# Kernel optimization log

Measured on AMD Instinct MI355X. Metric: run time of the kernel, lower is better.

Reference implementation:

```python
import jax, jax.numpy as jnp
import numpy as np

B, T, C, H = 8, 2048, 768, 64  # batch, seq_len, embedding_dim, head_size


def setup_inputs() -> dict:
    key = jax.random.key(0)
    k1, k2, k3, k4 = jax.random.split(key, 4)
    x = jax.random.normal(k1, (B, T, C), dtype=jnp.float32)
    attention_mask = jnp.ones((B, T), dtype=jnp.float32)
    # nn.Linear(C, H, bias=False) weights stored pre-transposed as (C, H)
    scale = 0.02
    Wq = jax.random.normal(k2, (C, H), dtype=jnp.float32) * scale
    Wk = jax.random.normal(k3, (C, H), dtype=jnp.float32) * scale
    Wv = jax.random.normal(k4, (C, H), dtype=jnp.float32) * scale
    return {"x": x, "attention_mask": attention_mask, "Wq": Wq, "Wk": Wk, "Wv": Wv}


def reference(x, attention_mask, Wq, Wk, Wv):
    # x: [B,T,C]; attention_mask: [B,T] (multiplied per query row)
    head_size = Wq.shape[-1]
    q = x @ Wq  # [B,T,H]
    k = x @ Wk  # [B,T,H]
    v = x @ Wv  # [B,T,H]
    inv_sqrt_h = jnp.asarray(1.0 / np.sqrt(head_size), x.dtype)
    s = jnp.einsum('bqh,bkh->bqk', q, k) * inv_sqrt_h  # [B,T,T]
    # attention_mask.unsqueeze(2) * qK ; masked_fill(qK == 0, -inf)
    s = attention_mask[:, :, None] * s
    s = jnp.where(s == 0, -jnp.inf, s)
    # causal tril mask
    seq = x.shape[1]
    tril = jnp.tril(jnp.ones((seq, seq), dtype=bool))
    s = jnp.where(tril[None, :, :], s, -jnp.inf)
    p = jax.nn.softmax(s, axis=-1)
    # dropout p=0.0 -> identity; nan cleanup (fully-masked rows)
    p = jnp.where(jnp.isnan(p), jnp.asarray(0.0, p.dtype), p)
    out = jnp.einsum('bqk,bkh->bqh', p, v)  # [B,T,H]
    return out
```

## Files before the change

kernel.cpp:

```cpp
#include <hip/hip_runtime.h>
#include <hip/hip_bf16.h>

#define B_ 8
#define T_ 2048
#define C_ 768
#define H_ 64
#define BT_ (B_*T_)

typedef __attribute__((ext_vector_type(8))) short bf16x8;
typedef __attribute__((ext_vector_type(4))) float f32x4;

__device__ __forceinline__ unsigned short f2bf(float x) {
    __hip_bfloat16 h = __float2bfloat16(x);
    return __builtin_bit_cast(unsigned short, h);
}

__device__ __forceinline__ bf16x8 cvt8(float4 a, float4 b) {
    bf16x8 r;
    r[0] = (short)f2bf(a.x); r[1] = (short)f2bf(a.y);
    r[2] = (short)f2bf(a.z); r[3] = (short)f2bf(a.w);
    r[4] = (short)f2bf(b.x); r[5] = (short)f2bf(b.y);
    r[6] = (short)f2bf(b.z); r[7] = (short)f2bf(b.w);
    return r;
}

__global__ __launch_bounds__(256) void wprep(
    const float* __restrict__ Wq, const float* __restrict__ Wk,
    const float* __restrict__ Wv, unsigned short* __restrict__ WTf)
{
    __shared__ float tile[32][68];
    const int bid = blockIdx.x;
    const int m = bid / 24, gc = bid % 24;
    const float* __restrict__ W = (m == 0) ? Wq : (m == 1) ? Wk : Wv;
    const int t = threadIdx.x;
    {
        const int r = t >> 3, c0 = (t & 7) * 8;
        float4 a = *(const float4*)(W + (size_t)(gc * 32 + r) * H_ + c0);
        float4 b = *(const float4*)(W + (size_t)(gc * 32 + r) * H_ + c0 + 4);
        *(float4*)&tile[r][c0]     = a;
        *(float4*)&tile[r][c0 + 4] = b;
    }
    __syncthreads();
    const int fl = t >> 6, lane = t & 63;
    const int q16 = lane & 15, quad = lane >> 4;
    const int f = m * 4 + fl;
    ushort4 u0, u1;
    u0.x = f2bf(tile[quad * 8 + 0][fl * 16 + q16]);
    u0.y = f2bf(tile[quad * 8 + 1][fl * 16 + q16]);
    u0.z = f2bf(tile[quad * 8 + 2][fl * 16 + q16]);
    u0.w = f2bf(tile[quad * 8 + 3][fl * 16 + q16]);
    u1.x = f2bf(tile[quad * 8 + 4][fl * 16 + q16]);
    u1.y = f2bf(tile[quad * 8 + 5][fl * 16 + q16]);
    u1.z = f2bf(tile[quad * 8 + 6][fl * 16 + q16]);
    u1.w = f2bf(tile[quad * 8 + 7][fl * 16 + q16]);
    unsigned short* __restrict__ dst = WTf + ((size_t)(gc * 12 + f) * 64 + lane) * 8;
    *(ushort4*)(dst)     = u0;
    *(ushort4*)(dst + 4) = u1;
}

__global__ __launch_bounds__(256) void qkv_kernel(
    const float* __restrict__ x, const unsigned short* __restrict__ WTf,
    unsigned short* __restrict__ qF, unsigned short* __restrict__ kF,
    unsigned short* __restrict__ vF)
{
    __shared__ __align__(16) unsigned short xS[16 * 772];
    const int tid  = threadIdx.x;
    const int w    = tid >> 6;
    const int lane = tid & 63;
    const int q16  = lane & 15, quad = lane >> 4;
    const int rowBase = blockIdx.x << 4;

    {
        const int r = tid >> 4, l = tid & 15;
        const float* __restrict__ xrow = x + (size_t)(rowBase + r) * C_;
        #pragma unroll
        for (int i = 0; i < 6; i++) {
            const int j = i * 16 + l;
            float4 a = *(const float4*)(xrow + j * 8);
            float4 b = *(const float4*)(xrow + j * 8 + 4);
            *(bf16x8*)&xS[(size_t)r * 772 + j * 8] = cvt8(a, b);
        }
    }
    __syncthreads();

    const int f0 = w * 3;
    const unsigned short* __restrict__ xrowS = xS + q16 * 772 + quad * 8;
    f32x4 acc[3] = {};
    #pragma unroll
    for (int c = 0; c < 24; c++) {
        const unsigned short* __restrict__ wpc =
            WTf + ((size_t)(c * 12 + f0)) * 512 + lane * 8;
        bf16x8 xf = *(const bf16x8*)(xrowS + c * 32);
        bf16x8 w0 = *(const bf16x8*)(wpc);
        bf16x8 w1 = *(const bf16x8*)(wpc + 512);
        bf16x8 w2 = *(const bf16x8*)(wpc + 1024);
        acc[0] = __builtin_amdgcn_mfma_f32_16x16x32_bf16(w0, xf, acc[0], 0, 0, 0);
        acc[1] = __builtin_amdgcn_mfma_f32_16x16x32_bf16(w1, xf, acc[1], 0, 0, 0);
        acc[2] = __builtin_amdgcn_mfma_f32_16x16x32_bf16(w2, xf, acc[2], 0, 0, 0);
    }

    const size_t gt = (size_t)(rowBase >> 4);
    #pragma unroll
    for (int j = 0; j < 3; j++) {
        const int f = f0 + j;
        if (f < 8) {
            ushort4 u;
            u.x = f2bf(acc[j][0]); u.y = f2bf(acc[j][1]);
            u.z = f2bf(acc[j][2]); u.w = f2bf(acc[j][3]);
            const int n4 = f & 3;
            const int qp = (2 * n4 + (quad >> 1)) & 3;
            const int j0 = (quad & 1) * 4;
            unsigned short* __restrict__ dst = (f < 4) ? qF : kF;
            *(ushort4*)(dst + ((gt * 2 + (n4 >> 1)) * 64 + q16 + 16 * qp) * 8 + j0) = u;
        } else {
            const size_t g32 = gt >> 1;
            const int qv = ((int)gt & 1) * 2 + (q16 >> 3);
            const int jv = q16 & 7;
            #pragma unroll
            for (int r = 0; r < 4; r++)
                vF[((g32 * 4 + (f - 8)) * 64 + quad * 4 + r + 16 * qv) * 8 + jv] =
                    f2bf(acc[j][r]);
        }
    }
}

__global__ __launch_bounds__(256) void attn_kernel(
    const unsigned short* __restrict__ qF, const unsigned short* __restrict__ kF,
    const unsigned short* __restrict__ vF, const float* __restrict__ mask,
    float* __restrict__ out)
{
    __shared__ __align__(16) unsigned short pS[4][16][88];
    __shared__ float oS[3][64][17];

    const int tid  = threadIdx.x;
    const int w    = tid >> 6;
    const int lane = tid & 63;
    const int q16  = lane & 15;
    const int quad = lane >> 4;
    const int bid  = blockIdx.x;
    const int b    = bid & 7;
    const int qt   = 127 - (bid >> 3);
    const int qrow = (qt << 4) + q16;

    const size_t qbase = ((size_t)(b * 128 + qt) * 2) * 512 + lane * 8;
    bf16x8 qf0 = *(const bf16x8*)(qF + qbase);
    bf16x8 qf1 = *(const bf16x8*)(qF + qbase + 512);
    const float mrow  = mask[b * T_ + qrow];
    const float maskv = mrow * 0.125f * 1.44269504f;

    f32x4 o[4] = {};
    float l_run = 0.f;

    const int niter = ((qt << 4) + 16 + 63) >> 6;
    const int dt    = niter - 1;

    bf16x8 kf[8], vf[8];
    auto loadK = [&](int kt_) {
        #pragma unroll
        for (int sub = 0; sub < 4; sub++) {
            const unsigned short* kp = kF + ((size_t)(b * 128 + kt_ * 4 + sub) * 2) * 512 + lane * 8;
            kf[2 * sub]     = *(const bf16x8*)(kp);
            kf[2 * sub + 1] = *(const bf16x8*)(kp + 512);
        }
    };
    auto loadV = [&](int kt_) {
        #pragma unroll
        for (int ht = 0; ht < 4; ht++) {
            const unsigned short* vp = vF + ((size_t)(b * 64 + kt_ * 2) * 4 + ht) * 512 + lane * 8;
            vf[2 * ht]     = *(const bf16x8*)(vp);
            vf[2 * ht + 1] = *(const bf16x8*)(vp + 4 * 512);
        }
    };

    if (w < niter) { loadK(w); loadV(w); }

    for (int kt = w; kt < niter; kt += 4) {
        const int kbase = kt << 6;
        const bool more = (kt + 4 < niter);

        f32x4 sa[4] = {};
        #pragma unroll
        for (int sub = 0; sub < 4; sub++) {
            sa[sub] = __builtin_amdgcn_mfma_f32_16x16x32_bf16(kf[2 * sub],     qf0, sa[sub], 0, 0, 0);
            sa[sub] = __builtin_amdgcn_mfma_f32_16x16x32_bf16(kf[2 * sub + 1], qf1, sa[sub], 0, 0, 0);
        }
        if (more) loadK(kt + 4);

        float p[16];
        if (kt != dt) {
            #pragma unroll
            for (int e = 0; e < 16; e++)
                p[e] = __builtin_amdgcn_exp2f(sa[e >> 2][e & 3] * maskv);
        } else {
            #pragma unroll
            for (int sub = 0; sub < 4; sub++)
                #pragma unroll
                for (int r = 0; r < 4; r++) {
                    int kidx = kbase + sub * 16 + quad * 4 + r;
                    float sv = sa[sub][r] * maskv;
                    sv = (kidx > qrow) ? -__builtin_inff() : sv;
                    p[sub * 4 + r] = __builtin_amdgcn_exp2f(sv);
                }
        }
        float psum = (((p[0] + p[1]) + (p[2] + p[3])) + ((p[4] + p[5]) + (p[6] + p[7])))
                   + (((p[8] + p[9]) + (p[10] + p[11])) + ((p[12] + p[13]) + (p[14] + p[15])));
        l_run += psum;

        #pragma unroll
        for (int sub = 0; sub < 4; sub++) {
            unsigned int lo = (unsigned int)f2bf(p[sub * 4 + 0]) | ((unsigned int)f2bf(p[sub * 4 + 1]) << 16);
            unsigned int hi = (unsigned int)f2bf(p[sub * 4 + 2]) | ((unsigned int)f2bf(p[sub * 4 + 3]) << 16);
            *(uint2*)&pS[w][q16][sub * 16 + quad * 4] = make_uint2(lo, hi);
        }
        bf16x8 pf0 = *(const bf16x8*)&pS[w][q16][quad * 8];
        bf16x8 pf1 = *(const bf16x8*)&pS[w][q16][32 + quad * 8];

        #pragma unroll
        for (int ht = 0; ht < 4; ht++) {
            o[ht] = __builtin_amdgcn_mfma_f32_16x16x32_bf16(vf[2 * ht],     pf0, o[ht], 0, 0, 0);
            o[ht] = __builtin_amdgcn_mfma_f32_16x16x32_bf16(vf[2 * ht + 1], pf1, o[ht], 0, 0, 0);
        }
        if (more) loadV(kt + 4);
    }

    l_run += __shfl_xor(l_run, 16);
    l_run += __shfl_xor(l_run, 32);

    if (w > 0) {
        #pragma unroll
        for (int ht = 0; ht < 4; ht++)
            #pragma unroll
            for (int r = 0; r < 4; r++) oS[w - 1][lane][ht * 4 + r] = o[ht][r];
        oS[w - 1][lane][16] = l_run;
    }
    __syncthreads();
    if (w == 0) {
        #pragma unroll
        for (int j = 0; j < 3; j++) {
            #pragma unroll
            for (int ht = 0; ht < 4; ht++)
                #pragma unroll
                for (int r = 0; r < 4; r++) o[ht][r] += oS[j][lane][ht * 4 + r];
            l_run += oS[j][lane][16];
        }
        const float invl = (mrow != 0.f && l_run > 0.f) ? (1.f / l_run) : 0.f;
        #pragma unroll
        for (int ht = 0; ht < 4; ht++) {
            float4 ov = make_float4(o[ht][0] * invl, o[ht][1] * invl,
                                    o[ht][2] * invl, o[ht][3] * invl);
            *(float4*)(out + ((size_t)(b * T_) + qrow) * H_ + ht * 16 + quad * 4) = ov;
        }
    }
}

extern "C" void kernel_launch(void* const* d_in, const int* in_sizes, int n_in,
                              void* d_out, int out_size, void* d_ws, size_t ws_size,
                              hipStream_t stream) {
    const float* x    = (const float*)d_in[0];
    const float* mask = (const float*)d_in[1];
    const float* Wq   = (const float*)d_in[2];
    const float* Wk   = (const float*)d_in[3];
    const float* Wv   = (const float*)d_in[4];
    float* out = (float*)d_out;

    unsigned short* qf = (unsigned short*)d_ws;
    unsigned short* kf = qf + (size_t)BT_ * H_;
    unsigned short* vf = kf + (size_t)BT_ * H_;
    unsigned short* wt = vf + (size_t)BT_ * H_;

    wprep<<<72, 256, 0, stream>>>(Wq, Wk, Wv, wt);
    qkv_kernel<<<BT_ / 16, 256, 0, stream>>>(x, wt, qf, kf, vf);
    attn_kernel<<<B_ * (T_ / 16), 256, 0, stream>>>(qf, kf, vf, mask, out);
}
```

Baseline: 114.8 us.

## Process two 16-row query tiles per block to reuse loaded K/V fragments

Each attention block now handles 32 query rows as two 16-row tiles (A and B) that share the same K and V fragments loaded per iteration, halving K/V global loads per query row. The grid shrinks to half as many blocks. The cost is more registers (two sets of accumulators and scores), fewer blocks for load balancing and occupancy, and tile A doing extra masked work up to tile B's causal length.

```diff
diff --git a/kernel.cpp b/kernel.cpp
--- a/kernel.cpp
+++ b/kernel.cpp
@@ -139,19 +139,26 @@
     const int quad = lane >> 4;
     const int bid  = blockIdx.x;
     const int b    = bid & 7;
-    const int qt   = 127 - (bid >> 3);
-    const int qrow = (qt << 4) + q16;
-
-    const size_t qbase = ((size_t)(b * 128 + qt) * 2) * 512 + lane * 8;
-    bf16x8 qf0 = *(const bf16x8*)(qF + qbase);
-    bf16x8 qf1 = *(const bf16x8*)(qF + qbase + 512);
-    const float mrow  = mask[b * T_ + qrow];
-    const float maskv = mrow * 0.125f * 1.44269504f;
-
-    f32x4 o[4] = {};
-    float l_run = 0.f;
-
-    const int niter = ((qt << 4) + 16 + 63) >> 6;
+    const int g    = 63 - (bid >> 3);
+    const int qtA  = 2 * g, qtB = 2 * g + 1;
+    const int qrowA = (qtA << 4) + q16;
+    const int qrowB = qrowA + 16;
+
+    const size_t qbaseA = ((size_t)(b * 128 + qtA) * 2) * 512 + lane * 8;
+    const size_t qbaseB = ((size_t)(b * 128 + qtB) * 2) * 512 + lane * 8;
+    bf16x8 qfA0 = *(const bf16x8*)(qF + qbaseA);
+    bf16x8 qfA1 = *(const bf16x8*)(qF + qbaseA + 512);
+    bf16x8 qfB0 = *(const bf16x8*)(qF + qbaseB);
+    bf16x8 qfB1 = *(const bf16x8*)(qF + qbaseB + 512);
+    const float mrowA  = mask[b * T_ + qrowA];
+    const float mrowB  = mask[b * T_ + qrowB];
+    const float maskvA = mrowA * 0.125f * 1.44269504f;
+    const float maskvB = mrowB * 0.125f * 1.44269504f;
+
+    f32x4 oA[4] = {}, oB[4] = {};
+    float lA = 0.f, lB = 0.f;
+
+    const int niter = ((qtB << 4) + 16 + 63) >> 6;
     const int dt    = niter - 1;
 
     bf16x8 kf[8], vf[8];
@@ -178,60 +185,122 @@
         const int kbase = kt << 6;
         const bool more = (kt + 4 < niter);
 
-        f32x4 sa[4] = {};
+        f32x4 saA[4] = {}, saB[4] = {};
         #pragma unroll
         for (int sub = 0; sub < 4; sub++) {
-            sa[sub] = __builtin_amdgcn_mfma_f32_16x16x32_bf16(kf[2 * sub],     qf0, sa[sub], 0, 0, 0);
-            sa[sub] = __builtin_amdgcn_mfma_f32_16x16x32_bf16(kf[2 * sub + 1], qf1, sa[sub], 0, 0, 0);
+            saA[sub] = __builtin_amdgcn_mfma_f32_16x16x32_bf16(kf[2 * sub],     qfA0, saA[sub], 0, 0, 0);
+            saA[sub] = __builtin_amdgcn_mfma_f32_16x16x32_bf16(kf[2 * sub + 1], qfA1, saA[sub], 0, 0, 0);
+            saB[sub] = __builtin_amdgcn_mfma_f32_16x16x32_bf16(kf[2 * sub],     qfB0, saB[sub], 0, 0, 0);
+            saB[sub] = __builtin_amdgcn_mfma_f32_16x16x32_bf16(kf[2 * sub + 1], qfB1, saB[sub], 0, 0, 0);
         }
         if (more) loadK(kt + 4);
 
-        float p[16];
-        if (kt != dt) {
-            #pragma unroll
-            for (int e = 0; e < 16; e++)
-                p[e] = __builtin_amdgcn_exp2f(sa[e >> 2][e & 3] * maskv);
-        } else {
-            #pragma unroll
-            for (int sub = 0; sub < 4; sub++)
-                #pragma unroll
-                for (int r = 0; r < 4; r++) {
-                    int kidx = kbase + sub * 16 + quad * 4 + r;
-                    float sv = sa[sub][r] * maskv;
-                    sv = (kidx > qrow) ? -__builtin_inff() : sv;
-                    p[sub * 4 + r] = __builtin_amdgcn_exp2f(sv);
-                }
-        }
-        float psum = (((p[0] + p[1]) + (p[2] + p[3])) + ((p[4] + p[5]) + (p[6] + p[7])))
-                   + (((p[8] + p[9]) + (p[10] + p[11])) + ((p[12] + p[13]) + (p[14] + p[15])));
-        l_run += psum;
-
-        #pragma unroll
-        for (int sub = 0; sub < 4; sub++) {
-            unsigned int lo = (unsigned int)f2bf(p[sub * 4 + 0]) | ((unsigned int)f2bf(p[sub * 4 + 1]) << 16);
-            unsigned int hi = (unsigned int)f2bf(p[sub * 4 + 2]) | ((unsigned int)f2bf(p[sub * 4 + 3]) << 16);
-            *(uint2*)&pS[w][q16][sub * 16 + quad * 4] = make_uint2(lo, hi);
-        }
-        bf16x8 pf0 = *(const bf16x8*)&pS[w][q16][quad * 8];
-        bf16x8 pf1 = *(const bf16x8*)&pS[w][q16][32 + quad * 8];
-
+        {
+            float p[16];
+            if (kt != dt) {
+                #pragma unroll
+                for (int e = 0; e < 16; e++)
+                    p[e] = __builtin_amdgcn_exp2f(saA[e >> 2][e & 3] * maskvA);
+            } else {
+                #pragma unroll
+                for (int sub = 0; sub < 4; sub++)
+                    #pragma unroll
+                    for (int r = 0; r < 4; r++) {
+                        int kidx = kbase + sub * 16 + quad * 4 + r;
+                        float sv = saA[sub][r] * maskvA;
+                        sv = (kidx > qrowA) ? -__builtin_inff() : sv;
+                        p[sub * 4 + r] = __builtin_amdgcn_exp2f(sv);
+                    }
+            }
+            lA += (((p[0] + p[1]) + (p[2] + p[3])) + ((p[4] + p[5]) + (p[6] + p[7])))
+                + (((p[8] + p[9]) + (p[10] + p[11])) + ((p[12] + p[13]) + (p[14] + p[15])));
+            #pragma unroll
+            for (int sub = 0; sub < 4; sub++) {
+                unsigned int lo = (unsigned int)f2bf(p[sub * 4 + 0]) | ((unsigned int)f2bf(p[sub * 4 + 1]) << 16);
+                unsigned int hi = (unsigned int)f2bf(p[sub * 4 + 2]) | ((unsigned int)f2bf(p[sub * 4 + 3]) << 16);
+                *(uint2*)&pS[w][q16][sub * 16 + quad * 4] = make_uint2(lo, hi);
+            }
+            bf16x8 pf0 = *(const bf16x8*)&pS[w][q16][quad * 8];
+            bf16x8 pf1 = *(const bf16x8*)&pS[w][q16][32 + quad * 8];
+            #pragma unroll
+            for (int ht = 0; ht < 4; ht++) {
+                oA[ht] = __builtin_amdgcn_mfma_f32_16x16x32_bf16(vf[2 * ht],     pf0, oA[ht], 0, 0, 0);
+                oA[ht] = __builtin_amdgcn_mfma_f32_16x16x32_bf16(vf[2 * ht + 1], pf1, oA[ht], 0, 0, 0);
+            }
+        }
+
+        {
+            float p[16];
+            if (kt != dt) {
+                #pragma unroll
+                for (int e = 0; e < 16; e++)
+                    p[e] = __builtin_amdgcn_exp2f(saB[e >> 2][e & 3] * maskvB);
+            } else {
+                #pragma unroll
+                for (int sub = 0; sub < 4; sub++)
+                    #pragma unroll
+                    for (int r = 0; r < 4; r++) {
+                        int kidx = kbase + sub * 16 + quad * 4 + r;
+                        float sv = saB[sub][r] * maskvB;
+                        sv = (kidx > qrowB) ? -__builtin_inff() : sv;
+                        p[sub * 4 + r] = __builtin_amdgcn_exp2f(sv);
+                    }
+            }
+            lB += (((p[0] + p[1]) + (p[2] + p[3])) + ((p[4] + p[5]) + (p[6] + p[7])))
+                + (((p[8] + p[9]) + (p[10] + p[11])) + ((p[12] + p[13]) + (p[14] + p[15])));
+            #pragma unroll
+            for (int sub = 0; sub < 4; sub++) {
+                unsigned int lo = (unsigned int)f2bf(p[sub * 4 + 0]) | ((unsigned int)f2bf(p[sub * 4 + 1]) << 16);
+                unsigned int hi = (unsigned int)f2bf(p[sub * 4 + 2]) | ((unsigned int)f2bf(p[sub * 4 + 3]) << 16);
+                *(uint2*)&pS[w][q16][sub * 16 + quad * 4] = make_uint2(lo, hi);
+            }
+            bf16x8 pf0 = *(const bf16x8*)&pS[w][q16][quad * 8];
+            bf16x8 pf1 = *(const bf16x8*)&pS[w][q16][32 + quad * 8];
+            #pragma unroll
+            for (int ht = 0; ht < 4; ht++) {
+                oB[ht] = __builtin_amdgcn_mfma_f32_16x16x32_bf16(vf[2 * ht],     pf0, oB[ht], 0, 0, 0);
+                oB[ht] = __builtin_amdgcn_mfma_f32_16x16x32_bf16(vf[2 * ht + 1], pf1, oB[ht], 0, 0, 0);
+            }
+        }
+        if (more) loadV(kt + 4);
+    }
+
+    lA += __shfl_xor(lA, 16); lA += __shfl_xor(lA, 32);
+    lB += __shfl_xor(lB, 16); lB += __shfl_xor(lB, 32);
+
+    if (w > 0) {
+        #pragma unroll
+        for (int ht = 0; ht < 4; ht++)
+            #pragma unroll
+            for (int r = 0; r < 4; r++) oS[w - 1][lane][ht * 4 + r] = oA[ht][r];
+        oS[w - 1][lane][16] = lA;
+    }
+    __syncthreads();
+    if (w == 0) {
+        #pragma unroll
+        for (int j = 0; j < 3; j++) {
+            #pragma unroll
+            for (int ht = 0; ht < 4; ht++)
+                #pragma unroll
+                for (int r = 0; r < 4; r++) oA[ht][r] += oS[j][lane][ht * 4 + r];
+            lA += oS[j][lane][16];
+        }
+        const float invl = (mrowA != 0.f && lA > 0.f) ? (1.f / lA) : 0.f;
         #pragma unroll
         for (int ht = 0; ht < 4; ht++) {
-            o[ht] = __builtin_amdgcn_mfma_f32_16x16x32_bf16(vf[2 * ht],     pf0, o[ht], 0, 0, 0);
-            o[ht] = __builtin_amdgcn_mfma_f32_16x16x32_bf16(vf[2 * ht + 1], pf1, o[ht], 0, 0, 0);
-        }
-        if (more) loadV(kt + 4);
-    }
-
-    l_run += __shfl_xor(l_run, 16);
-    l_run += __shfl_xor(l_run, 32);
+            float4 ov = make_float4(oA[ht][0] * invl, oA[ht][1] * invl,
+                                    oA[ht][2] * invl, oA[ht][3] * invl);
+            *(float4*)(out + ((size_t)(b * T_) + qrowA) * H_ + ht * 16 + quad * 4) = ov;
+        }
+    }
+    __syncthreads();
 
     if (w > 0) {
         #pragma unroll
         for (int ht = 0; ht < 4; ht++)
             #pragma unroll
-            for (int r = 0; r < 4; r++) oS[w - 1][lane][ht * 4 + r] = o[ht][r];
-        oS[w - 1][lane][16] = l_run;
+            for (int r = 0; r < 4; r++) oS[w - 1][lane][ht * 4 + r] = oB[ht][r];
+        oS[w - 1][lane][16] = lB;
     }
     __syncthreads();
     if (w == 0) {
@@ -240,15 +309,15 @@
             #pragma unroll
             for (int ht = 0; ht < 4; ht++)
                 #pragma unroll
-                for (int r = 0; r < 4; r++) o[ht][r] += oS[j][lane][ht * 4 + r];
-            l_run += oS[j][lane][16];
-        }
-        const float invl = (mrow != 0.f && l_run > 0.f) ? (1.f / l_run) : 0.f;
+                for (int r = 0; r < 4; r++) oB[ht][r] += oS[j][lane][ht * 4 + r];
+            lB += oS[j][lane][16];
+        }
+        const float invl = (mrowB != 0.f && lB > 0.f) ? (1.f / lB) : 0.f;
         #pragma unroll
         for (int ht = 0; ht < 4; ht++) {
-            float4 ov = make_float4(o[ht][0] * invl, o[ht][1] * invl,
-                                    o[ht][2] * invl, o[ht][3] * invl);
-            *(float4*)(out + ((size_t)(b * T_) + qrow) * H_ + ht * 16 + quad * 4) = ov;
+            float4 ov = make_float4(oB[ht][0] * invl, oB[ht][1] * invl,
+                                    oB[ht][2] * invl, oB[ht][3] * invl);
+            *(float4*)(out + ((size_t)(b * T_) + qrowB) * H_ + ht * 16 + quad * 4) = ov;
         }
     }
 }
@@ -270,5 +339,5 @@
 
     wprep<<<72, 256, 0, stream>>>(Wq, Wk, Wv, wt);
     qkv_kernel<<<BT_ / 16, 256, 0, stream>>>(x, wt, qf, kf, vf);
-    attn_kernel<<<B_ * (T_ / 16), 256, 0, stream>>>(qf, kf, vf, mask, out);
-}
+    attn_kernel<<<B_ * (T_ / 32), 256, 0, stream>>>(qf, kf, vf, mask, out);
+}
```

New measurement: 114.6 us. No clear change (-0.2%).
